# Kernel tuning notes

Hardware: AMD Instinct MI355X
Metric: run time of the kernel (lower is better)

The kernel has to match this reference:

```python
import jax, jax.numpy as jnp
import numpy as np


def _seq_shifts(n, max_len):
    # alternating-sign powers of two: [1,-1,2,-2,4,-4,...] capped by max_len
    shifts = []
    i = 0
    while len(shifts) < n and 2 ** i < max_len:
        shifts.append(2 ** i)
        if len(shifts) < n:
            shifts.append(-(2 ** i))
        i += 1
    return shifts

SPATIAL_SHIFTS = _seq_shifts(12, 2048)   # [1,-1,2,-2,4,-4,8,-8,16,-16,32,-32]
TEMPORAL_SHIFTS = _seq_shifts(4, 1 << 30)  # [1,-1,2,-2]
EPS = 1e-6


def setup_inputs() -> dict:
    key = jax.random.key(0)
    ks = jax.random.split(key, 8)
    B, L, C, H, D = 1, 8192, 1024, 16, 64
    inner = H * D
    w = 1.0 / np.sqrt(C)
    x = jax.random.normal(ks[0], (B, L, C), jnp.float32)
    Wq = jax.random.normal(ks[1], (C, inner), jnp.float32) * w
    Wk = jax.random.normal(ks[2], (C, inner), jnp.float32) * w
    Wv = jax.random.normal(ks[3], (C, inner), jnp.float32) * w
    Wo = jax.random.normal(ks[4], (inner, C), jnp.float32) * w
    bq = jnp.zeros((inner,), jnp.float32)
    bk = jnp.zeros((inner,), jnp.float32)
    bv = jnp.zeros((inner,), jnp.float32)
    bo = jnp.zeros((C,), jnp.float32)
    qn_w = jnp.ones((inner,), jnp.float32)
    kn_w = jnp.ones((inner,), jnp.float32)
    # edge bias initialized per the module's __init__ formula
    eb = np.zeros((H, len(SPATIAL_SHIFTS) + len(TEMPORAL_SHIFTS)), np.float32)
    for i, s in enumerate(SPATIAL_SHIFTS):
        eb[:, i] = 0.1 * np.log1p(abs(s))
    for i, s in enumerate(TEMPORAL_SHIFTS):
        eb[:, len(SPATIAL_SHIFTS) + i] = 0.2 * np.log1p(abs(s))
    edge_bias = jnp.asarray(eb)
    return {"x": x, "Wq": Wq, "bq": bq, "Wk": Wk, "bk": bk, "Wv": Wv, "bv": bv,
            "qn_w": qn_w, "kn_w": kn_w, "edge_bias": edge_bias, "Wo": Wo, "bo": bo,
            "num_frames": 8}


def _rms(t, w):
    return t * jax.lax.rsqrt(jnp.mean(t * t, axis=-1, keepdims=True) + EPS) * w


def reference(x, Wq, bq, Wk, bk, Wv, bv, qn_w, kn_w, edge_bias, Wo, bo, num_frames):
    B, L, _ = x.shape
    T = int(num_frames)
    S = L // T
    H, n_shifts = edge_bias.shape
    D = Wq.shape[1] // H
    scale = D ** -0.5
    msg = _rms(x @ Wq + bq, qn_w).reshape(B, T, S, H, D)
    key = _rms(x @ Wk + bk, kn_w).reshape(B, T, S, H, D)
    v5 = (x @ Wv + bv).reshape(B, T, S, H, D)
    scores, vals = [], []
    for s in SPATIAL_SHIFTS:  # neighbor idx (i+s)%S along spatial axis == roll(-s)
        k_nb = jnp.roll(key, -s, axis=2)
        vals.append(jnp.roll(v5, -s, axis=2))
        scores.append(jnp.einsum('btshd,btshd->btsh', msg, k_nb) * scale)
    for t in TEMPORAL_SHIFTS:  # neighbor idx (f+t)%T along frame axis
        k_nb = jnp.roll(key, -t, axis=1)
        vals.append(jnp.roll(v5, -t, axis=1))
        scores.append(jnp.einsum('btshd,btshd->btsh', msg, k_nb) * scale)
    sc = jnp.stack(scores, axis=-1) + edge_bias  # [B,T,S,H,N]
    attn = jax.nn.softmax(sc, axis=-1)
    v_stack = jnp.stack(vals, axis=-1)  # [B,T,S,H,D,N]
    out = jnp.einsum('btshn,btshdn->btshd', attn, v_stack).reshape(B, L, H * D)
    return out @ Wo + bo
```

## Files before the change

kernel.cpp:

```cpp
#include <hip/hip_runtime.h>
#include <hip/hip_bf16.h>

typedef __bf16 bf16x8 __attribute__((ext_vector_type(8)));
typedef float f32x4 __attribute__((ext_vector_type(4)));
typedef unsigned short ushort8 __attribute__((ext_vector_type(8)));
typedef unsigned short ushort_t;

#define AS3(p) ((__attribute__((address_space(3))) void*)(p))
#define AS1(p) ((const __attribute__((address_space(1))) void*)(p))

constexpr int L = 8192;
constexpr int C = 1024;
constexpr int T = 8;
constexpr int S = 1024;
constexpr int KT_C = 32;

__device__ __forceinline__ float bf2f(ushort_t u) {
    return __uint_as_float(((unsigned)u) << 16);
}
__device__ __forceinline__ ushort_t f2bf(float f) {
    unsigned x = __float_as_uint(f);
    unsigned r = (x + 0x7fffu + ((x >> 16) & 1u)) >> 16;
    return (ushort_t)r;
}

__global__ __launch_bounds__(256) void cvt_kernel(const float* __restrict__ in,
                                                  ushort_t* __restrict__ out, int n8) {
    int i = blockIdx.x * 256 + threadIdx.x;
    if (i >= n8) return;
    const float4* p = (const float4*)in + (long)i * 2;
    float4 a = p[0], b = p[1];
    ushort8 o;
    o[0] = f2bf(a.x); o[1] = f2bf(a.y); o[2] = f2bf(a.z); o[3] = f2bf(a.w);
    o[4] = f2bf(b.x); o[5] = f2bf(b.y); o[6] = f2bf(b.z); o[7] = f2bf(b.w);
    ((ushort8*)out)[i] = o;
}

__global__ __launch_bounds__(256) void transpose4_kernel(
    const float* __restrict__ w0, const float* __restrict__ w1,
    const float* __restrict__ w2, const float* __restrict__ w3,
    ushort_t* __restrict__ o0, ushort_t* __restrict__ o1,
    ushort_t* __restrict__ o2, ushort_t* __restrict__ o3) {
    int z = blockIdx.z;
    const float* W = z == 0 ? w0 : z == 1 ? w1 : z == 2 ? w2 : w3;
    ushort_t* O    = z == 0 ? o0 : z == 1 ? o1 : z == 2 ? o2 : o3;
    __shared__ float tile[32][33];
    int tx = threadIdx.x & 31, ty = threadIdx.x >> 5;
    int bx = blockIdx.x * 32, by = blockIdx.y * 32;
#pragma unroll
    for (int i = 0; i < 32; i += 8)
        tile[ty + i][tx] = W[(long)(by + ty + i) * C + bx + tx];
    __syncthreads();
#pragma unroll
    for (int i = 0; i < 32; i += 8)
        O[(long)(bx + ty + i) * C + by + tx] = f2bf(tile[tx][ty + i]);
}

#define VMW(n) asm volatile("s_waitcnt vmcnt(" #n ")" ::: "memory")

template <int OUT_MODE>
__device__ __forceinline__ void gemm256_body(const ushort_t* __restrict__ A,
                                             const ushort_t* __restrict__ Bt,
                                             const float* __restrict__ bias,
                                             void* __restrict__ Cv,
                                             int bx, int by) {
    __shared__ char lds[4 * 32768];
    const int tid = threadIdx.x;
    const int wave = tid >> 6, lane = tid & 63;
    const int wm = wave >> 2, wn = wave & 3;
    const long bm0 = (long)bx * 256, bn0 = (long)by * 256;

    const char* Ab = (const char*)A;
    const char* Bb = (const char*)Bt;
    long aSrc[2], bSrc[2];
#pragma unroll
    for (int j = 0; j < 2; j++) {
        int c = tid + j * 512, row = c >> 2, scol = (c & 3) ^ ((row >> 1) & 3);
        aSrc[j] = (bm0 + row) * (long)(C * 2) + scol * 16;
        bSrc[j] = (bn0 + row) * (long)(C * 2) + scol * 16;
    }
    const unsigned dOff = wave * 1024u;

#define STG(slot, it)                                                            \
    do {                                                                         \
        const long kb_ = (long)(it) * 64;                                        \
        char* s_ = lds + (slot) * 32768;                                         \
        __builtin_amdgcn_global_load_lds(AS1(Ab + aSrc[0] + kb_),                \
                                         AS3(s_ + dOff), 16, 0, 0);              \
        __builtin_amdgcn_global_load_lds(AS1(Ab + aSrc[1] + kb_),                \
                                         AS3(s_ + 8192 + dOff), 16, 0, 0);       \
        __builtin_amdgcn_global_load_lds(AS1(Bb + bSrc[0] + kb_),                \
                                         AS3(s_ + 16384 + dOff), 16, 0, 0);      \
        __builtin_amdgcn_global_load_lds(AS1(Bb + bSrc[1] + kb_),                \
                                         AS3(s_ + 24576 + dOff), 16, 0, 0);      \
    } while (0)

    const unsigned sl = ((lane >> 4) ^ ((lane >> 1) & 3)) * 16u;
    const unsigned rdA = (wm * 128 + (lane & 15)) * 64u + sl;
    const unsigned rdB = 16384u + (wn * 64 + (lane & 15)) * 64u + sl;

    f32x4 acc[8][4] = {};

    STG(0, 0); STG(1, 1); STG(2, 2);
    VMW(8);
    __builtin_amdgcn_s_barrier();

    for (int it = 0; it < KT_C; ++it) {
        if (it + 3 < KT_C) STG((it + 3) & 3, it + 3);
        const char* bs = lds + (it & 3) * 32768;
        bf16x8 af[8], bfr[4];
#pragma unroll
        for (int q = 0; q < 8; q++) af[q] = *(const bf16x8*)(bs + rdA + q * 1024);
#pragma unroll
        for (int j = 0; j < 4; j++) bfr[j] = *(const bf16x8*)(bs + rdB + j * 1024);

        __builtin_amdgcn_s_setprio(1);
#pragma unroll
        for (int q = 0; q < 8; q++)
#pragma unroll
            for (int j = 0; j < 4; j++)
                acc[q][j] = __builtin_amdgcn_mfma_f32_16x16x32_bf16(af[q], bfr[j],
                                                                    acc[q][j], 0, 0, 0);
        __builtin_amdgcn_s_setprio(0);

        if (it + 3 < KT_C)      { VMW(8); }
        else if (it + 2 < KT_C) { VMW(4); }
        else if (it + 1 < KT_C) { VMW(0); }
        if (it + 1 < KT_C) __builtin_amdgcn_s_barrier();
    }

    const int r0 = (int)bm0 + wm * 128 + (lane >> 4) * 4;
    const int c0 = (int)bn0 + wn * 64 + (lane & 15);
#pragma unroll
    for (int j = 0; j < 4; j++) {
        const int col = c0 + j * 16;
        const float bia = bias[col];
#pragma unroll
        for (int q = 0; q < 8; q++) {
            const int row = r0 + q * 16;
#pragma unroll
            for (int r = 0; r < 4; r++) {
                float val = acc[q][j][r] + bia;
                if (OUT_MODE == 1)
                    ((ushort_t*)Cv)[(size_t)(col >> 6) * (L * 64) +
                                    (long)(row + r) * 64 + (col & 63)] = f2bf(val);
                else
                    ((float*)Cv)[(long)(row + r) * C + col] = val;
            }
        }
    }
#undef STG
}

__global__ __launch_bounds__(512, 2) void gemm_qkv_kernel(
    const ushort_t* __restrict__ xbf,
    const ushort_t* __restrict__ WqT, const ushort_t* __restrict__ WkT,
    const ushort_t* __restrict__ WvT,
    const float* __restrict__ bq, const float* __restrict__ bk,
    const float* __restrict__ bv,
    ushort_t* __restrict__ q, ushort_t* __restrict__ k, ushort_t* __restrict__ v) {
    const int z = blockIdx.z;
    const ushort_t* Bt = z == 0 ? WqT : z == 1 ? WkT : WvT;
    const float* bias  = z == 0 ? bq : z == 1 ? bk : bv;
    ushort_t* out      = z == 0 ? q : z == 1 ? k : v;
    gemm256_body<1>(xbf, Bt, bias, out, blockIdx.x, blockIdx.y);
}

__global__ __launch_bounds__(512, 2) void gemm_o_kernel(
    const ushort_t* __restrict__ a, const ushort_t* __restrict__ WoT,
    const float* __restrict__ bo, float* __restrict__ outp) {
    gemm256_body<0>(a, WoT, bo, outp, blockIdx.x, blockIdx.y);
}

__global__ __launch_bounds__(256) void rownorm_kernel(
    const ushort_t* __restrict__ q, const ushort_t* __restrict__ k,
    float* __restrict__ rq, float* __restrict__ rk) {
    const int wave = threadIdx.x >> 6, lane = threadIdx.x & 63;
    const int p = blockIdx.x * 4 + wave;
    const int h = lane >> 2, qt = lane & 3;
    const size_t base = (size_t)h * (L * 64) + (long)p * 64 + qt * 16;
    const ushort8* qp = (const ushort8*)(q + base);
    const ushort8* kp = (const ushort8*)(k + base);
    ushort8 qa = qp[0], qb = qp[1], ka = kp[0], kb = kp[1];
    float sq = 0.f, sk = 0.f;
#pragma unroll
    for (int j = 0; j < 8; j++) {
        float a = bf2f(qa[j]), b = bf2f(qb[j]);
        sq += a * a + b * b;
        float c2 = bf2f(ka[j]), d = bf2f(kb[j]);
        sk += c2 * c2 + d * d;
    }
#pragma unroll
    for (int m = 1; m < 64; m <<= 1) { sq += __shfl_xor(sq, m); sk += __shfl_xor(sk, m); }
    if (lane == 0) {
        rq[p] = rsqrtf(sq * (1.0f / C) + 1e-6f);
        rk[p] = rsqrtf(sk * (1.0f / C) + 1e-6f);
    }
}

__global__ __launch_bounds__(256) void attn_kernel(
    const ushort_t* __restrict__ qraw, const ushort_t* __restrict__ kraw,
    const ushort_t* __restrict__ vraw,
    const float* __restrict__ qn_w, const float* __restrict__ kn_w,
    const float* __restrict__ eb, const float* __restrict__ rqA,
    const float* __restrict__ rkA, ushort_t* __restrict__ outp) {
    const int bid = blockIdx.x;
    const int t = bid & 7, chunk = (bid >> 3) & 31, h = bid >> 8;
    const int wave = threadIdx.x >> 6, lane = threadIdx.x & 63;
    const int pos = lane >> 3, cg = lane & 7;
    const int s = chunk * 32 + wave * 8 + pos;
    const int p = (t << 10) | s;

    const ushort_t* qb = qraw + (size_t)h * (L * 64);
    const ushort_t* kb = kraw + (size_t)h * (L * 64);
    const ushort_t* vb = vraw + (size_t)h * (L * 64);

    float qf[8];
    {
        ushort8 qv = *(const ushort8*)(qb + (long)p * 64 + cg * 8);
        const float rqv = rqA[p];
#pragma unroll
        for (int j = 0; j < 8; j++)
            qf[j] = bf2f(qv[j]) * rqv * qn_w[h * 64 + cg * 8 + j] * kn_w[h * 64 + cg * 8 + j];
    }

    const int SHF[16] = {1, -1, 2, -2, 4, -4, 8, -8, 16, -16, 32, -32, 1, -1, 2, -2};
    int pp[16];
#pragma unroll
    for (int n = 0; n < 16; n++) {
        if (n < 12) pp[n] = (t << 10) | ((s + SHF[n]) & (S - 1));
        else        pp[n] = (((t + SHF[n]) & (T - 1)) << 10) | s;
    }

    float sc[16];
#pragma unroll
    for (int n = 0; n < 16; n++) {
        ushort8 kv = *(const ushort8*)(kb + (long)pp[n] * 64 + cg * 8);
        float dot = 0.f;
#pragma unroll
        for (int j = 0; j < 8; j++) dot += qf[j] * bf2f(kv[j]);
        dot += __shfl_xor(dot, 1);
        dot += __shfl_xor(dot, 2);
        dot += __shfl_xor(dot, 4);
        sc[n] = dot * (rkA[pp[n]] * 0.125f) + eb[h * 16 + n];
    }

    float mx = sc[0];
#pragma unroll
    for (int n = 1; n < 16; n++) mx = fmaxf(mx, sc[n]);
    float wts[16], den = 0.f;
#pragma unroll
    for (int n = 0; n < 16; n++) { wts[n] = __expf(sc[n] - mx); den += wts[n]; }
    const float inv = 1.0f / den;

    float o[8] = {};
#pragma unroll
    for (int n = 0; n < 16; n++) {
        ushort8 vv = *(const ushort8*)(vb + (long)pp[n] * 64 + cg * 8);
#pragma unroll
        for (int j = 0; j < 8; j++) o[j] += wts[n] * bf2f(vv[j]);
    }

    ushort8 ov;
#pragma unroll
    for (int j = 0; j < 8; j++) ov[j] = f2bf(o[j] * inv);
    *(ushort8*)(outp + (long)p * C + h * 64 + cg * 8) = ov;
}

extern "C" void kernel_launch(void* const* d_in, const int* in_sizes, int n_in,
                              void* d_out, int out_size, void* d_ws, size_t ws_size,
                              hipStream_t stream) {
    const float* x    = (const float*)d_in[0];
    const float* Wq   = (const float*)d_in[1];
    const float* bq   = (const float*)d_in[2];
    const float* Wk   = (const float*)d_in[3];
    const float* bk   = (const float*)d_in[4];
    const float* Wv   = (const float*)d_in[5];
    const float* bv   = (const float*)d_in[6];
    const float* qn_w = (const float*)d_in[7];
    const float* kn_w = (const float*)d_in[8];
    const float* eb   = (const float*)d_in[9];
    const float* Wo   = (const float*)d_in[10];
    const float* bo   = (const float*)d_in[11];

    char* ws = (char*)d_ws;
    ushort_t* xbf  = (ushort_t*)ws;
    ushort_t* WqT  = (ushort_t*)(ws + (size_t)L * C * 2);
    ushort_t* WkT  = WqT + (size_t)C * C;
    ushort_t* WvT  = WkT + (size_t)C * C;
    ushort_t* WoT  = WvT + (size_t)C * C;
    ushort_t* qraw = WoT + (size_t)C * C;
    ushort_t* kraw = qraw + (size_t)L * C;
    ushort_t* vraw = kraw + (size_t)L * C;
    ushort_t* aout = vraw + (size_t)L * C;
    float* rqArr   = (float*)(aout + (size_t)L * C);
    float* rkArr   = rqArr + L;
    float* outp = (float*)d_out;

    cvt_kernel<<<(L * C / 8 + 255) / 256, 256, 0, stream>>>(x, xbf, L * C / 8);
    transpose4_kernel<<<dim3(32, 32, 4), 256, 0, stream>>>(Wq, Wk, Wv, Wo,
                                                           WqT, WkT, WvT, WoT);
    gemm_qkv_kernel<<<dim3(L / 256, C / 256, 3), 512, 0, stream>>>(
        xbf, WqT, WkT, WvT, bq, bk, bv, qraw, kraw, vraw);
    rownorm_kernel<<<L / 4, 256, 0, stream>>>(qraw, kraw, rqArr, rkArr);
    attn_kernel<<<T * 32 * 16, 256, 0, stream>>>(qraw, kraw, vraw, qn_w, kn_w, eb,
                                                 rqArr, rkArr, aout);
    gemm_o_kernel<<<dim3(L / 256, C / 256), 512, 0, stream>>>(aout, WoT, bo, outp);
}
```

Measured before the change: 276.4 us.

## Restructure GEMMs to 128x256 tiles with 4 waves and split-phase pipelining

```diff
diff --git a/kernel.cpp b/kernel.cpp
--- a/kernel.cpp
+++ b/kernel.cpp
@@ -57,80 +57,120 @@
 }
 
 #define VMW(n) asm volatile("s_waitcnt vmcnt(" #n ")" ::: "memory")
+#define GBAR() __builtin_amdgcn_s_barrier()
+#define LGKM0() asm volatile("s_waitcnt lgkmcnt(0)" ::: "memory")
 
 template <int OUT_MODE>
-__device__ __forceinline__ void gemm256_body(const ushort_t* __restrict__ A,
-                                             const ushort_t* __restrict__ Bt,
-                                             const float* __restrict__ bias,
-                                             void* __restrict__ Cv,
-                                             int bx, int by) {
-    __shared__ char lds[4 * 32768];
+__device__ __forceinline__ void gemm_body(const ushort_t* __restrict__ A,
+                                          const ushort_t* __restrict__ Bt,
+                                          const float* __restrict__ bias,
+                                          void* __restrict__ Cv,
+                                          int bx, int by) {
+    __shared__ char lds[3 * 24576];
     const int tid = threadIdx.x;
     const int wave = tid >> 6, lane = tid & 63;
-    const int wm = wave >> 2, wn = wave & 3;
-    const long bm0 = (long)bx * 256, bn0 = (long)by * 256;
+    const long bm0 = (long)bx * 128, bn0 = (long)by * 256;
 
     const char* Ab = (const char*)A;
     const char* Bb = (const char*)Bt;
-    long aSrc[2], bSrc[2];
+    long aSrc[2], bSrc[4];
 #pragma unroll
     for (int j = 0; j < 2; j++) {
-        int c = tid + j * 512, row = c >> 2, scol = (c & 3) ^ ((row >> 1) & 3);
+        int c = tid + j * 256, row = c >> 2, scol = (c & 3) ^ ((row >> 1) & 3);
         aSrc[j] = (bm0 + row) * (long)(C * 2) + scol * 16;
+    }
+#pragma unroll
+    for (int j = 0; j < 4; j++) {
+        int c = tid + j * 256, row = c >> 2, scol = (c & 3) ^ ((row >> 1) & 3);
         bSrc[j] = (bn0 + row) * (long)(C * 2) + scol * 16;
     }
-    const unsigned dOff = wave * 1024u;
-
-#define STG(slot, it)                                                            \
+    const unsigned wOff = wave * 1024u;
+
+#define STG_A(slot, itx)                                                         \
     do {                                                                         \
-        const long kb_ = (long)(it) * 64;                                        \
-        char* s_ = lds + (slot) * 32768;                                         \
+        const long kb_ = (long)(itx) * 64;                                       \
+        char* s_ = lds + (slot) * 24576;                                         \
         __builtin_amdgcn_global_load_lds(AS1(Ab + aSrc[0] + kb_),                \
-                                         AS3(s_ + dOff), 16, 0, 0);              \
+                                         AS3(s_ + wOff), 16, 0, 0);              \
         __builtin_amdgcn_global_load_lds(AS1(Ab + aSrc[1] + kb_),                \
-                                         AS3(s_ + 8192 + dOff), 16, 0, 0);       \
+                                         AS3(s_ + 4096 + wOff), 16, 0, 0);       \
+    } while (0)
+#define STG_B1(slot, itx)                                                        \
+    do {                                                                         \
+        const long kb_ = (long)(itx) * 64;                                       \
+        char* s_ = lds + (slot) * 24576;                                         \
         __builtin_amdgcn_global_load_lds(AS1(Bb + bSrc[0] + kb_),                \
-                                         AS3(s_ + 16384 + dOff), 16, 0, 0);      \
+                                         AS3(s_ + 8192 + wOff), 16, 0, 0);       \
+    } while (0)
+#define STG_B3(slot, itx)                                                        \
+    do {                                                                         \
+        const long kb_ = (long)(itx) * 64;                                       \
+        char* s_ = lds + (slot) * 24576;                                         \
         __builtin_amdgcn_global_load_lds(AS1(Bb + bSrc[1] + kb_),                \
-                                         AS3(s_ + 24576 + dOff), 16, 0, 0);      \
+                                         AS3(s_ + 12288 + wOff), 16, 0, 0);      \
+        __builtin_amdgcn_global_load_lds(AS1(Bb + bSrc[2] + kb_),                \
+                                         AS3(s_ + 16384 + wOff), 16, 0, 0);      \
+        __builtin_amdgcn_global_load_lds(AS1(Bb + bSrc[3] + kb_),                \
+                                         AS3(s_ + 20480 + wOff), 16, 0, 0);      \
     } while (0)
 
     const unsigned sl = ((lane >> 4) ^ ((lane >> 1) & 3)) * 16u;
-    const unsigned rdA = (wm * 128 + (lane & 15)) * 64u + sl;
-    const unsigned rdB = 16384u + (wn * 64 + (lane & 15)) * 64u + sl;
+    const unsigned rdA = (lane & 15) * 64u + sl;
+    const unsigned rdB = 8192u + (wave * 64 + (lane & 15)) * 64u + sl;
 
     f32x4 acc[8][4] = {};
-
-    STG(0, 0); STG(1, 1); STG(2, 2);
-    VMW(8);
-    __builtin_amdgcn_s_barrier();
-
+    bf16x8 af0[4], af1[4], bfr[4];
+
+    STG_A(0, 0); STG_B1(0, 0); STG_B3(0, 0);
+    STG_A(1, 1); STG_B1(1, 1); STG_B3(1, 1);
+    VMW(6);
+    GBAR();
+
+    int cs = 0;
     for (int it = 0; it < KT_C; ++it) {
-        if (it + 3 < KT_C) STG((it + 3) & 3, it + 3);
-        const char* bs = lds + (it & 3) * 32768;
-        bf16x8 af[8], bfr[4];
-#pragma unroll
-        for (int q = 0; q < 8; q++) af[q] = *(const bf16x8*)(bs + rdA + q * 1024);
+        const int s2 = (cs >= 1) ? cs - 1 : 2;
+        const char* bs = lds + cs * 24576;
+        const bool stg = (it + 2 < KT_C);
+
+#pragma unroll
+        for (int q = 0; q < 4; q++) af0[q] = *(const bf16x8*)(bs + rdA + q * 1024);
 #pragma unroll
         for (int j = 0; j < 4; j++) bfr[j] = *(const bf16x8*)(bs + rdB + j * 1024);
-
+        if (stg) { STG_A(s2, it + 2); STG_B1(s2, it + 2); }
+        GBAR();
+        LGKM0();
         __builtin_amdgcn_s_setprio(1);
 #pragma unroll
-        for (int q = 0; q < 8; q++)
+        for (int q = 0; q < 4; q++)
 #pragma unroll
             for (int j = 0; j < 4; j++)
-                acc[q][j] = __builtin_amdgcn_mfma_f32_16x16x32_bf16(af[q], bfr[j],
+                acc[q][j] = __builtin_amdgcn_mfma_f32_16x16x32_bf16(af0[q], bfr[j],
                                                                     acc[q][j], 0, 0, 0);
         __builtin_amdgcn_s_setprio(0);
-
-        if (it + 3 < KT_C)      { VMW(8); }
-        else if (it + 2 < KT_C) { VMW(4); }
-        else if (it + 1 < KT_C) { VMW(0); }
-        if (it + 1 < KT_C) __builtin_amdgcn_s_barrier();
-    }
-
-    const int r0 = (int)bm0 + wm * 128 + (lane >> 4) * 4;
-    const int c0 = (int)bn0 + wn * 64 + (lane & 15);
+        GBAR();
+
+#pragma unroll
+        for (int q = 0; q < 4; q++) af1[q] = *(const bf16x8*)(bs + rdA + (4 + q) * 1024);
+        if (stg) STG_B3(s2, it + 2);
+        GBAR();
+        LGKM0();
+        __builtin_amdgcn_s_setprio(1);
+#pragma unroll
+        for (int q = 0; q < 4; q++)
+#pragma unroll
+            for (int j = 0; j < 4; j++)
+                acc[4 + q][j] = __builtin_amdgcn_mfma_f32_16x16x32_bf16(af1[q], bfr[j],
+                                                                        acc[4 + q][j], 0, 0, 0);
+        __builtin_amdgcn_s_setprio(0);
+
+        if (stg)                 { VMW(6); }
+        else if (it + 1 < KT_C)  { VMW(0); }
+        if (it + 1 < KT_C) GBAR();
+        cs = (cs >= 2) ? 0 : cs + 1;
+    }
+
+    const int r0 = (int)bm0 + (lane >> 4) * 4;
+    const int c0 = (int)bn0 + wave * 64 + (lane & 15);
 #pragma unroll
     for (int j = 0; j < 4; j++) {
         const int col = c0 + j * 16;
@@ -149,10 +189,12 @@
             }
         }
     }
-#undef STG
-}
-
-__global__ __launch_bounds__(512, 2) void gemm_qkv_kernel(
+#undef STG_A
+#undef STG_B1
+#undef STG_B3
+}
+
+__global__ __launch_bounds__(256, 2) void gemm_qkv_kernel(
     const ushort_t* __restrict__ xbf,
     const ushort_t* __restrict__ WqT, const ushort_t* __restrict__ WkT,
     const ushort_t* __restrict__ WvT,
@@ -163,13 +205,13 @@
     const ushort_t* Bt = z == 0 ? WqT : z == 1 ? WkT : WvT;
     const float* bias  = z == 0 ? bq : z == 1 ? bk : bv;
     ushort_t* out      = z == 0 ? q : z == 1 ? k : v;
-    gemm256_body<1>(xbf, Bt, bias, out, blockIdx.x, blockIdx.y);
-}
-
-__global__ __launch_bounds__(512, 2) void gemm_o_kernel(
+    gemm_body<1>(xbf, Bt, bias, out, blockIdx.x, blockIdx.y);
+}
+
+__global__ __launch_bounds__(256, 2) void gemm_o_kernel(
     const ushort_t* __restrict__ a, const ushort_t* __restrict__ WoT,
     const float* __restrict__ bo, float* __restrict__ outp) {
-    gemm256_body<0>(a, WoT, bo, outp, blockIdx.x, blockIdx.y);
+    gemm_body<0>(a, WoT, bo, outp, blockIdx.x, blockIdx.y);
 }
 
 __global__ __launch_bounds__(256) void rownorm_kernel(
@@ -300,10 +342,10 @@
     cvt_kernel<<<(L * C / 8 + 255) / 256, 256, 0, stream>>>(x, xbf, L * C / 8);
     transpose4_kernel<<<dim3(32, 32, 4), 256, 0, stream>>>(Wq, Wk, Wv, Wo,
                                                            WqT, WkT, WvT, WoT);
-    gemm_qkv_kernel<<<dim3(L / 256, C / 256, 3), 512, 0, stream>>>(
+    gemm_qkv_kernel<<<dim3(L / 128, C / 256, 3), 256, 0, stream>>>(
         xbf, WqT, WkT, WvT, bq, bk, bv, qraw, kraw, vraw);
     rownorm_kernel<<<L / 4, 256, 0, stream>>>(qraw, kraw, rqArr, rkArr);
     attn_kernel<<<T * 32 * 16, 256, 0, stream>>>(qraw, kraw, vraw, qn_w, kn_w, eb,
                                                  rqArr, rkArr, aout);
-    gemm_o_kernel<<<dim3(L / 256, C / 256), 512, 0, stream>>>(aout, WoT, bo, outp);
-}
+    gemm_o_kernel<<<dim3(L / 128, C / 256), 256, 0, stream>>>(aout, WoT, bo, outp);
+}
```

Result: faster. 253.2 us (-8.4%).
